# Kernel tuning notes

Hardware: AMD Instinct MI355X
Metric: run time of the kernel (lower is better)

The kernel has to match this reference:

```python
import jax, jax.numpy as jnp
import numpy as np

HIDDEN = 2048
N_HEADS = 32
N_KV_HEADS = 8
HEAD_DIM = HIDDEN // N_HEADS  # 64
GROUPS = N_HEADS // N_KV_HEADS  # 4
ROPE_BASE = 10000.0


def _rope_cos_sin(seq_len, dim, dtype):
    inv_freq = 1.0 / (ROPE_BASE ** (jnp.arange(0, dim, 2, dtype=jnp.float32) / dim))
    t = jnp.arange(seq_len, dtype=jnp.float32)
    freqs = jnp.outer(t, inv_freq)            # [S, dim/2]
    emb = jnp.concatenate([freqs, freqs], -1)  # [S, dim]
    return jnp.cos(emb).astype(dtype), jnp.sin(emb).astype(dtype)


def _rotate_half(x):
    x1, x2 = jnp.split(x, 2, axis=-1)
    return jnp.concatenate([-x2, x1], axis=-1)


def setup_inputs() -> dict:
    key = jax.random.key(0)
    ks = jax.random.split(key, 5)
    x = jax.random.normal(ks[0], (2, 2048, HIDDEN), dtype=jnp.float32)
    scale = 0.02
    wq = jax.random.normal(ks[1], (HIDDEN, N_HEADS * HEAD_DIM), dtype=jnp.float32) * scale
    wk = jax.random.normal(ks[2], (HIDDEN, N_KV_HEADS * HEAD_DIM), dtype=jnp.float32) * scale
    wv = jax.random.normal(ks[3], (HIDDEN, N_KV_HEADS * HEAD_DIM), dtype=jnp.float32) * scale
    wo = jax.random.normal(ks[4], (N_HEADS * HEAD_DIM, HIDDEN), dtype=jnp.float32) * scale
    return {"x": x, "wq": wq, "wk": wk, "wv": wv, "wo": wo}


def reference(x, wq, wk, wv, wo):
    b, s, _ = x.shape
    # projections (torch Linear with weight stored transposed -> plain matmul here)
    q = (x @ wq).reshape(b, s, N_HEADS, HEAD_DIM).transpose(0, 2, 1, 3)      # [b,nh,s,d]
    k = (x @ wk).reshape(b, s, N_KV_HEADS, HEAD_DIM).transpose(0, 2, 1, 3)   # [b,kvh,s,d]
    v = (x @ wv).reshape(b, s, N_KV_HEADS, HEAD_DIM).transpose(0, 2, 1, 3)   # [b,kvh,s,d]

    cos, sin = _rope_cos_sin(s, HEAD_DIM, x.dtype)  # [s,d]
    cos = cos[None, None]  # [1,1,s,d]
    sin = sin[None, None]
    q = q * cos + _rotate_half(q) * sin
    k = k * cos + _rotate_half(k) * sin

    # GQA: group query heads per KV head instead of expanding K/V
    qg = q.reshape(b, N_KV_HEADS, GROUPS, s, HEAD_DIM)
    scores = jnp.einsum('bhgqd,bhkd->bhgqk', qg, k) / np.sqrt(HEAD_DIM).astype(x.dtype)
    probs = jax.nn.softmax(scores.astype(jnp.float32), axis=-1).astype(x.dtype)
    out = jnp.einsum('bhgqk,bhkd->bhgqd', probs, v)          # [b,kvh,g,s,d]
    out = out.reshape(b, N_HEADS, s, HEAD_DIM).transpose(0, 2, 1, 3).reshape(b, s, HIDDEN)
    return out @ wo
```

## Files before the change

kernel.cpp:

```cpp
#include <hip/hip_runtime.h>


typedef __bf16 bf16;
typedef __bf16 bf16x4_t __attribute__((ext_vector_type(4)));
typedef __bf16 bf16x8_t __attribute__((ext_vector_type(8)));
typedef float  f32x4_t  __attribute__((ext_vector_type(4)));
typedef unsigned int u32;
typedef unsigned int u32x4_t __attribute__((ext_vector_type(4)));

#define S_LEN 2048
#define HID   2048
#define NH    32
#define KVH   8
#define HD    64

__device__ __forceinline__ void async_copy16(const void* g, void* l) {
  __builtin_amdgcn_global_load_lds(
      (const __attribute__((address_space(1))) void*)g,
      (__attribute__((address_space(3))) void*)l, 16, 0, 0);
}

__device__ __forceinline__ u32 cvt_pk_bf16(float lo, float hi) {
  u32 r;
  asm("v_cvt_pk_bf16_f32 %0, %1, %2" : "=v"(r) : "v"(lo), "v"(hi));
  return r;
}

__device__ __forceinline__ void permlane32_swap(u32& a, u32& b) {
  asm("v_permlane32_swap_b32 %0, %1" : "+v"(a), "+v"(b));
}

__global__ __launch_bounds__(256) void cast_bf16_kernel(
    const float* __restrict__ src, bf16* __restrict__ dst) {
  int i = (blockIdx.x * 256 + threadIdx.x) * 4;
  float4 v = *(const float4*)(src + i);
  bf16x4_t o;
  o[0] = (bf16)v.x; o[1] = (bf16)v.y; o[2] = (bf16)v.z; o[3] = (bf16)v.w;
  *(bf16x4_t*)(dst + i) = o;
}

__global__ __launch_bounds__(256) void wtrans_kernel(
    const float* __restrict__ src, bf16* __restrict__ dst, int C, int dstStride) {
  __shared__ float tile[32][33];
  int c0 = blockIdx.x * 32, r0 = blockIdx.y * 32;
  int t = threadIdx.x;
  int r = t >> 3, c4 = (t & 7) * 4;
  float4 v = *(const float4*)(src + (size_t)(r0 + r) * C + c0 + c4);
  tile[r][c4] = v.x; tile[r][c4 + 1] = v.y; tile[r][c4 + 2] = v.z; tile[r][c4 + 3] = v.w;
  __syncthreads();
  int cc = t >> 3, r4 = (t & 7) * 4;
  bf16x4_t o;
  o[0] = (bf16)tile[r4][cc];     o[1] = (bf16)tile[r4 + 1][cc];
  o[2] = (bf16)tile[r4 + 2][cc]; o[3] = (bf16)tile[r4 + 3][cc];
  *(bf16x4_t*)(dst + (size_t)(c0 + cc) * dstStride + r0 + r4) = o;
}

__global__ __launch_bounds__(256, 2) void qkv_gemm_rope(
    const bf16* __restrict__ A, const bf16* __restrict__ Bt,
    bf16* __restrict__ q_r, bf16* __restrict__ k_r, bf16* __restrict__ v_t) {
  __shared__ char smem[32768];
  char* As = smem;
  char* Bs = smem + 16384;
  const int tid  = threadIdx.x;
  const int wid  = tid >> 6;
  const int lane = tid & 63;
  const int l15  = lane & 15;
  const int quad = lane >> 4;
  const int wm = wid >> 1, wn = wid & 1;
  const int bm = blockIdx.y * 128;
  const int bn = blockIdx.x * 128;
  const int K = 2048;

  f32x4_t acc[4][4] = {};

  for (int k0 = 0; k0 < K; k0 += 64) {
#pragma unroll
    for (int it = 0; it < 4; ++it) {
      int p = it * 256 + tid;
      int row = p >> 3;
      int j = (p & 7) ^ (row & 7);
      async_copy16(A + (size_t)(bm + row) * K + k0 + j * 8,
                   As + (size_t)(it * 256 + wid * 64) * 16);
      async_copy16(Bt + (size_t)(bn + row) * K + k0 + j * 8,
                   Bs + (size_t)(it * 256 + wid * 64) * 16);
    }
    __syncthreads();
#pragma unroll
    for (int kk = 0; kk < 64; kk += 32) {
      bf16x8_t af[4], bfr[4];
      int cbase = (kk >> 3) + quad;
#pragma unroll
      for (int mt = 0; mt < 4; ++mt) {
        int row = wm * 64 + mt * 16 + l15;
        af[mt] = *(const bf16x8_t*)(As + (size_t)(row * 8 + (cbase ^ (row & 7))) * 16);
      }
#pragma unroll
      for (int nt = 0; nt < 4; ++nt) {
        int row = wn * 64 + nt * 16 + l15;
        bfr[nt] = *(const bf16x8_t*)(Bs + (size_t)(row * 8 + (cbase ^ (row & 7))) * 16);
      }
#pragma unroll
      for (int mt = 0; mt < 4; ++mt)
#pragma unroll
        for (int nt = 0; nt < 4; ++nt)
          acc[mt][nt] = __builtin_amdgcn_mfma_f32_16x16x32_bf16(
              af[mt], bfr[nt], acc[mt][nt], 0, 0, 0);
    }
    __syncthreads();
  }

  const int cb = blockIdx.x * 2 + wn;
  const int rowbase = bm + wm * 64;
  const int bidx = bm >> 11;
  const float LE = 0.41524101186098285f;
  const float SC = 0.18033688011112043f;

  if (cb < 40) {
    const bool isQ = (cb < 32);
    const float sc = isQ ? SC : 1.0f;
    bf16* base = isQ ? (q_r + (size_t)(bidx * NH + cb) * S_LEN * HD)
                     : (k_r + (size_t)(bidx * KVH + (cb - 32)) * S_LEN * HD);
#pragma unroll
    for (int nt = 0; nt < 2; ++nt) {
      int i = nt * 16 + l15;
      float inv = __builtin_exp2f(-(float)i * LE);
#pragma unroll
      for (int mt = 0; mt < 4; ++mt)
#pragma unroll
        for (int r = 0; r < 4; ++r) {
          int row = rowbase + mt * 16 + quad * 4 + r;
          int s = row & 2047;
          float ang = (float)s * inv;
          float sv, cv;
          __sincosf(ang, &sv, &cv);
          float x1 = acc[mt][nt][r], x2 = acc[mt][nt + 2][r];
          bf16* d = base + (size_t)s * HD;
          d[i]      = (bf16)((x1 * cv - x2 * sv) * sc);
          d[i + 32] = (bf16)((x2 * cv + x1 * sv) * sc);
        }
    }
  } else {
    const int kvh = cb - 40;
    bf16* base = v_t + (size_t)(bidx * KVH + kvh) * HD * S_LEN;
#pragma unroll
    for (int nt = 0; nt < 4; ++nt) {
      int d = nt * 16 + l15;
#pragma unroll
      for (int mt = 0; mt < 4; ++mt) {
        int s0 = (rowbase + mt * 16 + quad * 4) & 2047;
        bf16x4_t o;
        o[0] = (bf16)acc[mt][nt][0]; o[1] = (bf16)acc[mt][nt][1];
        o[2] = (bf16)acc[mt][nt][2]; o[3] = (bf16)acc[mt][nt][3];
        *(bf16x4_t*)(base + (size_t)d * S_LEN + s0) = o;
      }
    }
  }
}

template <typename OutT>
__global__ __launch_bounds__(256, 2) void gemm_bt(
    const bf16* __restrict__ A, const bf16* __restrict__ Bt,
    OutT* __restrict__ C, int N, int K) {
  __shared__ char smem[32768];
  char* As = smem;
  char* Bs = smem + 16384;
  const int tid  = threadIdx.x;
  const int wid  = tid >> 6;
  const int lane = tid & 63;
  const int l15  = lane & 15;
  const int quad = lane >> 4;
  const int wm = wid >> 1, wn = wid & 1;
  const int bm = blockIdx.y * 128;
  const int bn = blockIdx.x * 128;

  f32x4_t acc[4][4] = {};

  for (int k0 = 0; k0 < K; k0 += 64) {
#pragma unroll
    for (int it = 0; it < 4; ++it) {
      int p = it * 256 + tid;
      int row = p >> 3;
      int j = (p & 7) ^ (row & 7);
      async_copy16(A + (size_t)(bm + row) * K + k0 + j * 8,
                   As + (size_t)(it * 256 + wid * 64) * 16);
      async_copy16(Bt + (size_t)(bn + row) * K + k0 + j * 8,
                   Bs + (size_t)(it * 256 + wid * 64) * 16);
    }
    __syncthreads();
#pragma unroll
    for (int kk = 0; kk < 64; kk += 32) {
      bf16x8_t af[4], bfr[4];
      int cbase = (kk >> 3) + quad;
#pragma unroll
      for (int mt = 0; mt < 4; ++mt) {
        int row = wm * 64 + mt * 16 + l15;
        af[mt] = *(const bf16x8_t*)(As + (size_t)(row * 8 + (cbase ^ (row & 7))) * 16);
      }
#pragma unroll
      for (int nt = 0; nt < 4; ++nt) {
        int row = wn * 64 + nt * 16 + l15;
        bfr[nt] = *(const bf16x8_t*)(Bs + (size_t)(row * 8 + (cbase ^ (row & 7))) * 16);
      }
#pragma unroll
      for (int mt = 0; mt < 4; ++mt)
#pragma unroll
        for (int nt = 0; nt < 4; ++nt)
          acc[mt][nt] = __builtin_amdgcn_mfma_f32_16x16x32_bf16(
              af[mt], bfr[nt], acc[mt][nt], 0, 0, 0);
    }
    __syncthreads();
  }
#pragma unroll
  for (int mt = 0; mt < 4; ++mt)
#pragma unroll
    for (int nt = 0; nt < 4; ++nt)
#pragma unroll
      for (int r = 0; r < 4; ++r) {
        int row = bm + wm * 64 + mt * 16 + quad * 4 + r;
        int col = bn + wn * 64 + nt * 16 + l15;
        C[(size_t)row * N + col] = (OutT)acc[mt][nt][r];
      }
}

__global__ __launch_bounds__(256, 4) void attn_kernel(
    const bf16* __restrict__ q_r, const bf16* __restrict__ k_r,
    const bf16* __restrict__ v_t, bf16* __restrict__ attn) {
  __shared__ char smem[32768];
  char* Ks = smem;
  char* Vs = smem + 16384;
  const int tid = threadIdx.x;
  const int wid = tid >> 6;
  const int lane = tid & 63;
  const int l15 = lane & 15, quad = lane >> 4;

  const int lin = blockIdx.x + (blockIdx.y << 7);
  const int xcd = lin & 7;
  const int w = lin >> 3;
  const int blky = xcd * 2 + (w >> 7);
  const int q0 = (w & 127) * 16;

  const int b = blky >> 3, kvh = blky & 7;
  const int h = kvh * 4 + wid;

  const bf16* Kg = k_r + (size_t)blky * S_LEN * HD;
  const bf16* Vg = v_t + (size_t)blky * HD * S_LEN;

  bf16x8_t qf0, qf1;
  {
    const bf16* qb = q_r + ((size_t)(b * NH + h) * S_LEN + q0 + l15) * HD;
    qf0 = *(const bf16x8_t*)(qb + quad * 8);
    qf1 = *(const bf16x8_t*)(qb + 32 + quad * 8);
  }
  bf16x8_t ones;
#pragma unroll
  for (int e = 0; e < 8; ++e) ones[e] = (bf16)1.0f;

  f32x4_t o_acc[4] = {};
  f32x4_t l_acc = {};

#pragma unroll
  for (int it = 0; it < 4; ++it) {
    int p = it * 256 + tid;
    int row = p >> 3, j = (p & 7) ^ (row & 7);
    int gr = (row & ~12) | ((row & 4) << 1) | ((row & 8) >> 1);
    async_copy16(Kg + (size_t)gr * HD + j * 8,
                 Ks + (size_t)(it * 256 + wid * 64) * 16);
  }

  for (int kt = 0; kt < S_LEN / 128; ++kt) {
    __syncthreads();
#pragma unroll
    for (int it = 0; it < 4; ++it) {
      int p = it * 256 + tid;
      int vrow = p >> 4, vj = (p & 15) ^ (vrow & 15);
      async_copy16(Vg + (size_t)vrow * S_LEN + kt * 128 + vj * 8,
                   Vs + (size_t)(it * 256 + wid * 64) * 16);
    }

    bf16x8_t pf[4];
    {
      f32x4_t sa[8];
#pragma unroll
      for (int t = 0; t < 8; ++t) sa[t] = f32x4_t{0.f, 0.f, 0.f, 0.f};
#pragma unroll
      for (int t = 0; t < 8; ++t) {
        int row = t * 16 + l15;
        int s3 = l15 & 7;
        bf16x8_t kf0 = *(const bf16x8_t*)(Ks + (size_t)(row * 8 + (quad ^ s3)) * 16);
        bf16x8_t kf1 = *(const bf16x8_t*)(Ks + (size_t)(row * 8 + ((4 + quad) ^ s3)) * 16);
        sa[t] = __builtin_amdgcn_mfma_f32_16x16x32_bf16(kf0, qf0, sa[t], 0, 0, 0);
        sa[t] = __builtin_amdgcn_mfma_f32_16x16x32_bf16(kf1, qf1, sa[t], 0, 0, 0);
      }
#pragma unroll
      for (int c = 0; c < 4; ++c) {
        u32 w0 = cvt_pk_bf16(__builtin_exp2f(sa[2 * c][0]),
                             __builtin_exp2f(sa[2 * c][1]));
        u32 w1 = cvt_pk_bf16(__builtin_exp2f(sa[2 * c][2]),
                             __builtin_exp2f(sa[2 * c][3]));
        u32 w2 = cvt_pk_bf16(__builtin_exp2f(sa[2 * c + 1][0]),
                             __builtin_exp2f(sa[2 * c + 1][1]));
        u32 w3 = cvt_pk_bf16(__builtin_exp2f(sa[2 * c + 1][2]),
                             __builtin_exp2f(sa[2 * c + 1][3]));
        permlane32_swap(w0, w2);
        permlane32_swap(w1, w3);
        u32x4_t pw;
        pw[0] = w0; pw[1] = w1; pw[2] = w2; pw[3] = w3;
        pf[c] = __builtin_bit_cast(bf16x8_t, pw);
      }
    }

    __syncthreads();

    if (kt < S_LEN / 128 - 1) {
#pragma unroll
      for (int it = 0; it < 4; ++it) {
        int p = it * 256 + tid;
        int row = p >> 3, j = (p & 7) ^ (row & 7);
        int gr = (row & ~12) | ((row & 4) << 1) | ((row & 8) >> 1);
        async_copy16(Kg + (size_t)((kt + 1) * 128 + gr) * HD + j * 8,
                     Ks + (size_t)(it * 256 + wid * 64) * 16);
      }
    }

#pragma unroll
    for (int c = 0; c < 4; ++c) {
      l_acc = __builtin_amdgcn_mfma_f32_16x16x32_bf16(ones, pf[c], l_acc, 0, 0, 0);
#pragma unroll
      for (int nt = 0; nt < 4; ++nt) {
        int d = nt * 16 + l15;
        bf16x8_t vf = *(const bf16x8_t*)(Vs + d * 256 + (((4 * c + quad) ^ l15) * 16));
        o_acc[nt] = __builtin_amdgcn_mfma_f32_16x16x32_bf16(vf, pf[c], o_acc[nt], 0, 0, 0);
      }
    }
  }

  char* Pw = smem + wid * 4096;
  {
    float inv = 1.0f / l_acc[0];
#pragma unroll
    for (int nt = 0; nt < 4; ++nt) {
      bf16x4_t o;
      o[0] = (bf16)(o_acc[nt][0] * inv);
      o[1] = (bf16)(o_acc[nt][1] * inv);
      o[2] = (bf16)(o_acc[nt][2] * inv);
      o[3] = (bf16)(o_acc[nt][3] * inv);
      *(bf16x4_t*)(Pw + l15 * 144 + (nt * 16 + quad * 4) * 2) = o;
    }
    int row = lane >> 2, cc = lane & 3;
    bf16x8_t r0 = *(const bf16x8_t*)(Pw + row * 144 + cc * 32);
    bf16x8_t r1 = *(const bf16x8_t*)(Pw + row * 144 + cc * 32 + 16);
    int token = q0 + row;
    bf16* dst = attn + ((size_t)(b * S_LEN + token)) * HID + h * 64 + cc * 16;
    *(bf16x8_t*)dst = r0;
    *(bf16x8_t*)(dst + 8) = r1;
  }
}

extern "C" void kernel_launch(void* const* d_in, const int* in_sizes, int n_in,
                              void* d_out, int out_size, void* d_ws, size_t ws_size,
                              hipStream_t stream) {
  const float* x  = (const float*)d_in[0];
  const float* wq = (const float*)d_in[1];
  const float* wk = (const float*)d_in[2];
  const float* wv = (const float*)d_in[3];
  const float* wo = (const float*)d_in[4];
  float* out = (float*)d_out;
  char* ws = (char*)d_ws;

  bf16* q_r    = (bf16*)(ws + 0);
  bf16* k_r    = (bf16*)(ws + 16777216);
  bf16* v_t    = (bf16*)(ws + 20971520);
  bf16* wqkv_t = (bf16*)(ws + 25165824);
  bf16* attn   = (bf16*)(ws + 25165824);
  bf16* wo_t   = (bf16*)(ws + 16777216);
  bf16* x_b    = (bf16*)d_out;

  cast_bf16_kernel<<<8192, 256, 0, stream>>>(x, x_b);
  wtrans_kernel<<<dim3(64, 64), 256, 0, stream>>>(wq, wqkv_t, 2048, 2048);
  wtrans_kernel<<<dim3(16, 64), 256, 0, stream>>>(wk, wqkv_t + (size_t)2048 * 2048, 512, 2048);
  wtrans_kernel<<<dim3(16, 64), 256, 0, stream>>>(wv, wqkv_t + (size_t)2560 * 2048, 512, 2048);

  qkv_gemm_rope<<<dim3(24, 32), 256, 0, stream>>>(x_b, wqkv_t, q_r, k_r, v_t);
  attn_kernel<<<dim3(128, 16), 256, 0, stream>>>(q_r, k_r, v_t, attn);

  wtrans_kernel<<<dim3(64, 64), 256, 0, stream>>>(wo, wo_t, 2048, 2048);
  gemm_bt<float><<<dim3(16, 32), 256, 0, stream>>>(attn, wo_t, out, 2048, 2048);
}
```

Measured before the change: 327.6 us.

## Precompute RoPE table, double attention block to 512 threads, add MFMA priority hints

Precomputes the RoPE cos/sin table inside the cast kernel and has the QKV GEMM epilogue read it instead of calling sincos per element. The attention kernel now runs 8 waves per block covering 32 queries, so each K/V tile in LDS is shared by twice as many query rows and the number of blocks is halved. It also raises wave priority around the MFMA sections and adds a barrier before LDS is reused for the output. The risks are extra global traffic for the rope table, fewer blocks per CU, and heavier register and LDS pressure under the 512-thread launch bound.

```diff
diff --git a/kernel.cpp b/kernel.cpp
--- a/kernel.cpp
+++ b/kernel.cpp
@@ -31,12 +31,23 @@
 }
 
 __global__ __launch_bounds__(256) void cast_bf16_kernel(
-    const float* __restrict__ src, bf16* __restrict__ dst) {
-  int i = (blockIdx.x * 256 + threadIdx.x) * 4;
+    const float* __restrict__ src, bf16* __restrict__ dst,
+    float2* __restrict__ rope) {
+  int gid = blockIdx.x * 256 + threadIdx.x;
+  int i = gid * 4;
   float4 v = *(const float4*)(src + i);
   bf16x4_t o;
   o[0] = (bf16)v.x; o[1] = (bf16)v.y; o[2] = (bf16)v.z; o[3] = (bf16)v.w;
   *(bf16x4_t*)(dst + i) = o;
+  if (gid < S_LEN * 32) {
+    int s = gid >> 5, fi = gid & 31;
+    const float LE = 0.41524101186098285f;
+    float inv = __builtin_exp2f(-(float)fi * LE);
+    float ang = (float)s * inv;
+    float sv, cv;
+    __sincosf(ang, &sv, &cv);
+    rope[gid] = make_float2(cv, sv);
+  }
 }
 
 __global__ __launch_bounds__(256) void wtrans_kernel(
@@ -57,7 +68,8 @@
 
 __global__ __launch_bounds__(256, 2) void qkv_gemm_rope(
     const bf16* __restrict__ A, const bf16* __restrict__ Bt,
-    bf16* __restrict__ q_r, bf16* __restrict__ k_r, bf16* __restrict__ v_t) {
+    bf16* __restrict__ q_r, bf16* __restrict__ k_r, bf16* __restrict__ v_t,
+    const float2* __restrict__ rope) {
   __shared__ char smem[32768];
   char* As = smem;
   char* Bs = smem + 16384;
@@ -112,7 +124,6 @@
   const int cb = blockIdx.x * 2 + wn;
   const int rowbase = bm + wm * 64;
   const int bidx = bm >> 11;
-  const float LE = 0.41524101186098285f;
   const float SC = 0.18033688011112043f;
 
   if (cb < 40) {
@@ -123,20 +134,17 @@
 #pragma unroll
     for (int nt = 0; nt < 2; ++nt) {
       int i = nt * 16 + l15;
-      float inv = __builtin_exp2f(-(float)i * LE);
 #pragma unroll
       for (int mt = 0; mt < 4; ++mt)
 #pragma unroll
         for (int r = 0; r < 4; ++r) {
           int row = rowbase + mt * 16 + quad * 4 + r;
           int s = row & 2047;
-          float ang = (float)s * inv;
-          float sv, cv;
-          __sincosf(ang, &sv, &cv);
+          float2 cs = rope[s * 32 + i];
           float x1 = acc[mt][nt][r], x2 = acc[mt][nt + 2][r];
           bf16* d = base + (size_t)s * HD;
-          d[i]      = (bf16)((x1 * cv - x2 * sv) * sc);
-          d[i + 32] = (bf16)((x2 * cv + x1 * sv) * sc);
+          d[i]      = (bf16)((x1 * cs.x - x2 * cs.y) * sc);
+          d[i + 32] = (bf16)((x2 * cs.x + x1 * cs.y) * sc);
         }
     }
   } else {
@@ -222,7 +230,7 @@
       }
 }
 
-__global__ __launch_bounds__(256, 4) void attn_kernel(
+__global__ __launch_bounds__(512, 8) void attn_kernel(
     const bf16* __restrict__ q_r, const bf16* __restrict__ k_r,
     const bf16* __restrict__ v_t, bf16* __restrict__ attn) {
   __shared__ char smem[32768];
@@ -233,14 +241,14 @@
   const int lane = tid & 63;
   const int l15 = lane & 15, quad = lane >> 4;
 
-  const int lin = blockIdx.x + (blockIdx.y << 7);
+  const int lin = blockIdx.x + (blockIdx.y << 6);
   const int xcd = lin & 7;
   const int w = lin >> 3;
-  const int blky = xcd * 2 + (w >> 7);
-  const int q0 = (w & 127) * 16;
+  const int blky = xcd * 2 + (w >> 6);
+  const int q0 = (w & 63) * 32 + (wid >> 2) * 16;
 
   const int b = blky >> 3, kvh = blky & 7;
-  const int h = kvh * 4 + wid;
+  const int h = kvh * 4 + (wid & 3);
 
   const bf16* Kg = k_r + (size_t)blky * S_LEN * HD;
   const bf16* Vg = v_t + (size_t)blky * HD * S_LEN;
@@ -259,22 +267,22 @@
   f32x4_t l_acc = {};
 
 #pragma unroll
-  for (int it = 0; it < 4; ++it) {
-    int p = it * 256 + tid;
+  for (int it = 0; it < 2; ++it) {
+    int p = it * 512 + tid;
     int row = p >> 3, j = (p & 7) ^ (row & 7);
     int gr = (row & ~12) | ((row & 4) << 1) | ((row & 8) >> 1);
     async_copy16(Kg + (size_t)gr * HD + j * 8,
-                 Ks + (size_t)(it * 256 + wid * 64) * 16);
+                 Ks + (size_t)(it * 512 + wid * 64) * 16);
   }
 
   for (int kt = 0; kt < S_LEN / 128; ++kt) {
     __syncthreads();
 #pragma unroll
-    for (int it = 0; it < 4; ++it) {
-      int p = it * 256 + tid;
+    for (int it = 0; it < 2; ++it) {
+      int p = it * 512 + tid;
       int vrow = p >> 4, vj = (p & 15) ^ (vrow & 15);
       async_copy16(Vg + (size_t)vrow * S_LEN + kt * 128 + vj * 8,
-                   Vs + (size_t)(it * 256 + wid * 64) * 16);
+                   Vs + (size_t)(it * 512 + wid * 64) * 16);
     }
 
     bf16x8_t pf[4];
@@ -282,6 +290,7 @@
       f32x4_t sa[8];
 #pragma unroll
       for (int t = 0; t < 8; ++t) sa[t] = f32x4_t{0.f, 0.f, 0.f, 0.f};
+      __builtin_amdgcn_s_setprio(1);
 #pragma unroll
       for (int t = 0; t < 8; ++t) {
         int row = t * 16 + l15;
@@ -291,6 +300,7 @@
         sa[t] = __builtin_amdgcn_mfma_f32_16x16x32_bf16(kf0, qf0, sa[t], 0, 0, 0);
         sa[t] = __builtin_amdgcn_mfma_f32_16x16x32_bf16(kf1, qf1, sa[t], 0, 0, 0);
       }
+      __builtin_amdgcn_s_setprio(0);
 #pragma unroll
       for (int c = 0; c < 4; ++c) {
         u32 w0 = cvt_pk_bf16(__builtin_exp2f(sa[2 * c][0]),
@@ -313,15 +323,16 @@
 
     if (kt < S_LEN / 128 - 1) {
 #pragma unroll
-      for (int it = 0; it < 4; ++it) {
-        int p = it * 256 + tid;
+      for (int it = 0; it < 2; ++it) {
+        int p = it * 512 + tid;
         int row = p >> 3, j = (p & 7) ^ (row & 7);
         int gr = (row & ~12) | ((row & 4) << 1) | ((row & 8) >> 1);
         async_copy16(Kg + (size_t)((kt + 1) * 128 + gr) * HD + j * 8,
-                     Ks + (size_t)(it * 256 + wid * 64) * 16);
-      }
-    }
-
+                     Ks + (size_t)(it * 512 + wid * 64) * 16);
+      }
+    }
+
+    __builtin_amdgcn_s_setprio(1);
 #pragma unroll
     for (int c = 0; c < 4; ++c) {
       l_acc = __builtin_amdgcn_mfma_f32_16x16x32_bf16(ones, pf[c], l_acc, 0, 0, 0);
@@ -332,8 +343,10 @@
         o_acc[nt] = __builtin_amdgcn_mfma_f32_16x16x32_bf16(vf, pf[c], o_acc[nt], 0, 0, 0);
       }
     }
-  }
-
+    __builtin_amdgcn_s_setprio(0);
+  }
+
+  __syncthreads();
   char* Pw = smem + wid * 4096;
   {
     float inv = 1.0f / l_acc[0];
@@ -373,15 +386,16 @@
   bf16* wqkv_t = (bf16*)(ws + 25165824);
   bf16* attn   = (bf16*)(ws + 25165824);
   bf16* wo_t   = (bf16*)(ws + 16777216);
+  float2* rope = (float2*)(ws + 37748736);
   bf16* x_b    = (bf16*)d_out;
 
-  cast_bf16_kernel<<<8192, 256, 0, stream>>>(x, x_b);
+  cast_bf16_kernel<<<8192, 256, 0, stream>>>(x, x_b, rope);
   wtrans_kernel<<<dim3(64, 64), 256, 0, stream>>>(wq, wqkv_t, 2048, 2048);
   wtrans_kernel<<<dim3(16, 64), 256, 0, stream>>>(wk, wqkv_t + (size_t)2048 * 2048, 512, 2048);
   wtrans_kernel<<<dim3(16, 64), 256, 0, stream>>>(wv, wqkv_t + (size_t)2560 * 2048, 512, 2048);
 
-  qkv_gemm_rope<<<dim3(24, 32), 256, 0, stream>>>(x_b, wqkv_t, q_r, k_r, v_t);
-  attn_kernel<<<dim3(128, 16), 256, 0, stream>>>(q_r, k_r, v_t, attn);
+  qkv_gemm_rope<<<dim3(24, 32), 256, 0, stream>>>(x_b, wqkv_t, q_r, k_r, v_t, rope);
+  attn_kernel<<<dim3(64, 16), 512, 0, stream>>>(q_r, k_r, v_t, attn);
 
   wtrans_kernel<<<dim3(64, 64), 256, 0, stream>>>(wo, wo_t, 2048, 2048);
   gemm_bt<float><<<dim3(16, 32), 256, 0, stream>>>(attn, wo_t, out, 2048, 2048);
```

New measurement: 518.5 us. +58.3%, slower.
